# Kernel optimization log

Hardware: AMD Instinct MI355X
Metric: run time of the kernel (lower is better)

The kernel has to match this reference:

```python
import jax, jax.numpy as jnp
import numpy as np

H = 256   # input_size
P = 256   # state_size
BATCH, L = 8, 4096
DT_MIN, DT_MAX = 1e-3, 1e-1
LN_EPS = 1e-5


def _hippo_params():
    # HiPPO-N matrix (num_blocks=1), eigendecomposition in numpy (float64 then cast)
    idx = np.arange(P, dtype=np.float64)
    s = np.sqrt(idx + 0.5)
    A = -np.outer(s, s)
    A = np.tril(A) - np.triu(A, 1)
    np.fill_diagonal(A, -0.5)
    ev, V = np.linalg.eig(A)
    order = np.argsort(ev.real)
    ev, V = ev[order], V[:, order]
    return ev, V


def setup_inputs() -> dict:
    key = jax.random.key(0)
    k_u, = jax.random.split(key, 1)
    ev, V = _hippo_params()
    rng = np.random.default_rng(0)
    log_lambda_real = np.log(-np.clip(ev.real, None, -1e-4)).astype(np.float32)
    lambda_imag = ev.imag.astype(np.float32)
    V_inv = np.linalg.inv(V)
    B_init = rng.standard_normal((P, H)) / np.sqrt(P)
    B_tilde = V_inv @ B_init.astype(np.complex128)
    C_init = rng.standard_normal((H, P)) / np.sqrt(P)
    C_tilde = C_init.astype(np.complex128) @ V
    log_delta = (rng.random(P) * (np.log(DT_MAX) - np.log(DT_MIN)) + np.log(DT_MIN)).astype(np.float32)
    return {
        "u": jax.random.normal(k_u, (BATCH, L, H), dtype=jnp.float32),
        "log_lambda_real": jnp.asarray(log_lambda_real),
        "lambda_imag": jnp.asarray(lambda_imag),
        "B_tilde_real": jnp.asarray(B_tilde.real, dtype=jnp.float32),
        "B_tilde_imag": jnp.asarray(B_tilde.imag, dtype=jnp.float32),
        "C_tilde_real": jnp.asarray(C_tilde.real, dtype=jnp.float32),
        "C_tilde_imag": jnp.asarray(C_tilde.imag, dtype=jnp.float32),
        "log_delta": jnp.asarray(log_delta),
        "gamma": jnp.ones((H,), dtype=jnp.float32),
        "beta": jnp.zeros((H,), dtype=jnp.float32),
    }


def _layernorm(x, gamma, beta):
    mu = jnp.mean(x, axis=-1, keepdims=True)
    var = jnp.mean(jnp.square(x - mu), axis=-1, keepdims=True)
    return (x - mu) * jax.lax.rsqrt(var + LN_EPS) * gamma + beta


def _ssm(h, log_lambda_real, lambda_imag, B_tilde_real, B_tilde_imag,
         C_tilde_real, C_tilde_imag, log_delta):
    # Continuous-time diagonal SSM params
    lam = -jnp.exp(log_lambda_real) + 1j * lambda_imag            # (P,) complex
    B_tilde = B_tilde_real + 1j * B_tilde_imag                     # (P,H)
    C_tilde = C_tilde_real + 1j * C_tilde_imag                     # (H,P)
    delta = jnp.exp(log_delta)                                     # (P,)
    # ZOH discretization (eq. 6 of the S5 paper)
    lambda_bar = jnp.exp(lam * delta)                              # (P,)
    B_bar = ((lambda_bar - 1.0) / lam)[:, None] * B_tilde          # (P,H)
    # Bu_k = B_bar @ u_k  ->  (B,L,P) complex
    Bu = jnp.einsum('blh,ph->blp', h.astype(jnp.complex64), B_bar.astype(jnp.complex64))
    # Parallel associative scan for x_k = lambda_bar * x_{k-1} + Bu_k
    a = jnp.broadcast_to(lambda_bar.astype(jnp.complex64), Bu.shape)
    def combine(c1, c2):
        a1, b1 = c1
        a2, b2 = c2
        return a1 * a2, a2 * b1 + b2
    _, xs = jax.lax.associative_scan(combine, (a, Bu), axis=1)     # (B,L,P)
    # Project back to real output: y = Re(C_tilde @ x)
    y = jnp.einsum('blp,hp->blh', xs, C_tilde.astype(jnp.complex64)).real
    return y


def reference(u, log_lambda_real, lambda_imag, B_tilde_real, B_tilde_imag,
              C_tilde_real, C_tilde_imag, log_delta, gamma, beta):
    # S5Block: pre-LayerNorm -> S5 SSM -> GELU -> residual
    h = _layernorm(u, gamma, beta)
    y = _ssm(h, log_lambda_real, lambda_imag, B_tilde_real, B_tilde_imag,
             C_tilde_real, C_tilde_imag, log_delta)
    return u + jax.nn.gelu(y)
```

## Files before the change

### kernel.cpp

```cpp
#include <hip/hip_runtime.h>
#include <math.h>

#define HDIM 256
#define PDIM 256
#define BATCH 8
#define LSEQ 4096
#define MTOT (BATCH * LSEQ)
#define CHLEN 128
#define NCHUNK 32

typedef __attribute__((ext_vector_type(8))) short bf16x8;
typedef __attribute__((ext_vector_type(4))) float f32x4;

__device__ __forceinline__ unsigned short f2bf(float f) {
    union { float f; unsigned int u; } v; v.f = f;
    unsigned int r = v.u + 0x7FFFu + ((v.u >> 16) & 1u);
    return (unsigned short)(r >> 16);
}
__device__ __forceinline__ float bf2f(unsigned int lo16) {
    union { unsigned int u; float f; } v; v.u = lo16 << 16;
    return v.f;
}

__global__ void prep_k(const float* __restrict__ Br, const float* __restrict__ Bi,
                       const float* __restrict__ Cr, const float* __restrict__ Ci,
                       const float* __restrict__ llr, const float* __restrict__ lim,
                       const float* __restrict__ ldl,
                       unsigned short* __restrict__ W1t, unsigned short* __restrict__ W2t,
                       float* __restrict__ par, float* __restrict__ apw) {
    int p = blockIdx.x, h = threadIdx.x;
    float er = expf(llr[p]);
    float im = lim[p];
    float d  = expf(ldl[p]);
    float zr = -er * d, zi = im * d;
    float ea = expf(zr);
    float ar = ea * cosf(zi), ai = ea * sinf(zi);
    float dr = -er, di = im;
    float den = dr * dr + di * di;
    float nr = ar - 1.0f, ni = ai;
    float cr = (nr * dr + ni * di) / den;
    float ci = (ni * dr - nr * di) / den;
    float br = Br[p * HDIM + h], bi = Bi[p * HDIM + h];
    W1t[(2 * p) * HDIM + h]     = f2bf(cr * br - ci * bi);
    W1t[(2 * p + 1) * HDIM + h] = f2bf(cr * bi + ci * br);
    W2t[h * 512 + 2 * p]     = f2bf(Cr[h * PDIM + p]);
    W2t[h * 512 + 2 * p + 1] = f2bf(-Ci[h * PDIM + p]);
    if (h == 0) {
        par[2 * p]     = ar;
        par[2 * p + 1] = ai;
        float pr = ar, pi = ai;
        apw[2 * p] = pr; apw[2 * p + 1] = pi;
        for (int j = 1; j < CHLEN; j++) {
            float tr = pr * ar - pi * ai;
            float ti = pr * ai + pi * ar;
            pr = tr; pi = ti;
            apw[j * 512 + 2 * p]     = pr;
            apw[j * 512 + 2 * p + 1] = pi;
        }
    }
}

__global__ void ln_k(const float* __restrict__ u, unsigned short* __restrict__ hbf,
                     const float* __restrict__ gamma, const float* __restrict__ beta) {
    __shared__ float gS[HDIM], bS[HDIM];
    int t = threadIdx.x;
    gS[t] = gamma[t]; bS[t] = beta[t];
    int lane = t & 63, wv = t >> 6;
    int row = blockIdx.x * 4 + wv;
    float4 v = *(const float4*)(u + (size_t)row * HDIM + lane * 4);
    float s  = v.x + v.y + v.z + v.w;
    float sq = v.x * v.x + v.y * v.y + v.z * v.z + v.w * v.w;
    #pragma unroll
    for (int o = 1; o < 64; o <<= 1) { s += __shfl_xor(s, o); sq += __shfl_xor(sq, o); }
    float mu = s * (1.0f / HDIM);
    float rs = rsqrtf(sq * (1.0f / HDIM) - mu * mu + 1e-5f);
    __syncthreads();
    int c = lane * 4;
    ushort4 o;
    o.x = f2bf((v.x - mu) * rs * gS[c + 0] + bS[c + 0]);
    o.y = f2bf((v.y - mu) * rs * gS[c + 1] + bS[c + 1]);
    o.z = f2bf((v.z - mu) * rs * gS[c + 2] + bS[c + 2]);
    o.w = f2bf((v.w - mu) * rs * gS[c + 3] + bS[c + 3]);
    *(ushort4*)(hbf + (size_t)row * HDIM + c) = o;
}

__launch_bounds__(256, 2)
__global__ void gemm1_k(const unsigned short* __restrict__ A, const unsigned short* __restrict__ B,
                        unsigned short* __restrict__ Bu, float* __restrict__ last,
                        const float* __restrict__ par, const float* __restrict__ apw) {
    __shared__ union {
        struct { unsigned short A[128 * 32]; unsigned short B[128 * 32]; } st;
        unsigned short C[128 * 128];
    } sm;

    const int t = threadIdx.x;
    const int bn = blockIdx.x, bm = blockIdx.y;
    const int lane = t & 63;
    const int wm = ((t >> 6) & 1) * 64;
    const int wn = ((t >> 6) >> 1) * 64;
    const int srow = t >> 1, skoff = (t & 1) * 16;
    const unsigned short* Ap = A + (size_t)(bm * 128 + srow) * 256 + skoff;
    const unsigned short* Bp = B + (size_t)(bn * 128 + srow) * 256 + skoff;
    const int mrow = lane & 15, kq = (lane >> 4) * 8;

    f32x4 acc[4][4] = {};

    for (int k0 = 0; k0 < 256; k0 += 32) {
        uint4 a0 = *(const uint4*)(Ap + k0);
        uint4 a1 = *(const uint4*)(Ap + k0 + 8);
        uint4 b0 = *(const uint4*)(Bp + k0);
        uint4 b1 = *(const uint4*)(Bp + k0 + 8);
        __syncthreads();
        *(uint4*)&sm.st.A[srow * 32 + skoff]     = a0;
        *(uint4*)&sm.st.A[srow * 32 + skoff + 8] = a1;
        *(uint4*)&sm.st.B[srow * 32 + skoff]     = b0;
        *(uint4*)&sm.st.B[srow * 32 + skoff + 8] = b1;
        __syncthreads();
        bf16x8 fa[4], fb[4];
        #pragma unroll
        for (int i = 0; i < 4; i++) {
            fa[i] = *(const bf16x8*)&sm.st.A[(wm + i * 16 + mrow) * 32 + kq];
            fb[i] = *(const bf16x8*)&sm.st.B[(wn + i * 16 + mrow) * 32 + kq];
        }
        #pragma unroll
        for (int i = 0; i < 4; i++)
            #pragma unroll
            for (int j = 0; j < 4; j++)
                acc[i][j] = __builtin_amdgcn_mfma_f32_16x16x32_bf16(fa[i], fb[j], acc[i][j], 0, 0, 0);
    }

    __syncthreads();
    const int r0 = (lane >> 4) * 4, c0 = lane & 15;
    #pragma unroll
    for (int i = 0; i < 4; i++)
        #pragma unroll
        for (int j = 0; j < 4; j++)
            #pragma unroll
            for (int r = 0; r < 4; r++)
                sm.C[(wm + i * 16 + r0 + r) * 128 + wn + j * 16 + c0] = f2bf(acc[i][j][r]);
    __syncthreads();

    if (t < 64) {
        int pg = bn * 64 + t;
        float ar = par[2 * pg], ai = par[2 * pg + 1];
        float xr = 0.0f, xi = 0.0f;
        unsigned int* Cw = (unsigned int*)sm.C;
        #pragma unroll 8
        for (int s = 0; s < CHLEN; s++) {
            unsigned int v = Cw[s * 64 + t];
            float vr = bf2f(v & 0xFFFFu), vi = bf2f(v >> 16);
            float nr = fmaf(ar, xr, fmaf(-ai, xi, vr));
            float ni = fmaf(ar, xi, fmaf(ai, xr, vi));
            xr = nr; xi = ni;
            Cw[s * 64 + t] = (unsigned int)f2bf(xr) | ((unsigned int)f2bf(xi) << 16);
        }
        *(float2*)(last + (size_t)(bm * 256 + pg) * 2) = make_float2(xr, xi);
    }
    __syncthreads();

    {
        int row = t >> 1, ch = (t & 1) * 64;
        unsigned short* dst = Bu + (size_t)(bm * 128 + row) * 512 + bn * 128 + ch;
        const unsigned short* src = &sm.C[row * 128 + ch];
        #pragma unroll
        for (int q = 0; q < 8; q++)
            *(uint4*)(dst + q * 8) = *(const uint4*)(src + q * 8);
    }
}

__global__ void carry_k(const float* __restrict__ last, float* __restrict__ prefix,
                        const float* __restrict__ apw) {
    int p = threadIdx.x, b = blockIdx.x;
    float Ar = apw[127 * 512 + 2 * p], Ai = apw[127 * 512 + 2 * p + 1];
    float Pr = 0.0f, Pi = 0.0f;
    for (int c = 0; c < NCHUNK; c++) {
        size_t idx = (size_t)((b * NCHUNK + c) * 256 + p) * 2;
        *(float2*)(prefix + idx) = make_float2(Pr, Pi);
        float2 l = *(const float2*)(last + idx);
        float nr = fmaf(Ar, Pr, fmaf(-Ai, Pi, l.x));
        float ni = fmaf(Ar, Pi, fmaf(Ai, Pr, l.y));
        Pr = nr; Pi = ni;
    }
}

__global__ void apply_k(unsigned short* __restrict__ Bu, const float* __restrict__ apw,
                        const float* __restrict__ prefix) {
    int c = blockIdx.x;
    if (c == 0) return;
    int b = blockIdx.y;
    int t = threadIdx.x;
    int k = t & 255;
    int j0 = (t >> 8) * 64;
    float2 P = *(const float2*)(prefix + ((size_t)(b * NCHUNK + c) * 256 + k) * 2);
    unsigned int* q = (unsigned int*)(Bu + ((size_t)b * LSEQ + (size_t)c * CHLEN + j0) * 512) + k;
    const float2* ap = (const float2*)apw + (size_t)j0 * 256 + k;
    #pragma unroll 4
    for (int j = 0; j < 64; j++) {
        float2 a2 = ap[(size_t)j * 256];
        unsigned int v = q[(size_t)j * 256];
        float vr = bf2f(v & 0xFFFFu), vi = bf2f(v >> 16);
        float xr = fmaf(a2.x, P.x, fmaf(-a2.y, P.y, vr));
        float xi = fmaf(a2.x, P.y, fmaf(a2.y, P.x, vi));
        q[(size_t)j * 256] = (unsigned int)f2bf(xr) | ((unsigned int)f2bf(xi) << 16);
    }
}

#define LDK 40
__launch_bounds__(256, 2)
__global__ void gemm2_k(const unsigned short* __restrict__ A, const unsigned short* __restrict__ B,
                        float* __restrict__ out, const float* __restrict__ u) {
    __shared__ unsigned short As[128 * LDK];
    __shared__ unsigned short Bs[128 * LDK];
    const int t = threadIdx.x;
    const int bn = blockIdx.x, bm = blockIdx.y;
    const int lane = t & 63;
    const int wm = ((t >> 6) & 1) * 64;
    const int wn = ((t >> 6) >> 1) * 64;
    const int srow = t >> 1, skoff = (t & 1) * 16;
    const unsigned short* Ap = A + (size_t)(bm * 128 + srow) * 512 + skoff;
    const unsigned short* Bp = B + (size_t)(bn * 128 + srow) * 512 + skoff;
    unsigned short* AsW = &As[srow * LDK + skoff];
    unsigned short* BsW = &Bs[srow * LDK + skoff];
    const int mrow = lane & 15, kq = (lane >> 4) * 8;

    f32x4 acc[4][4] = {};

    for (int k0 = 0; k0 < 512; k0 += 32) {
        uint4 a0 = *(const uint4*)(Ap + k0);
        uint4 a1 = *(const uint4*)(Ap + k0 + 8);
        uint4 b0 = *(const uint4*)(Bp + k0);
        uint4 b1 = *(const uint4*)(Bp + k0 + 8);
        __syncthreads();
        *(uint4*)AsW       = a0;
        *(uint4*)(AsW + 8) = a1;
        *(uint4*)BsW       = b0;
        *(uint4*)(BsW + 8) = b1;
        __syncthreads();
        bf16x8 fa[4], fb[4];
        #pragma unroll
        for (int i = 0; i < 4; i++) {
            fa[i] = *(const bf16x8*)&As[(wm + i * 16 + mrow) * LDK + kq];
            fb[i] = *(const bf16x8*)&Bs[(wn + i * 16 + mrow) * LDK + kq];
        }
        #pragma unroll
        for (int i = 0; i < 4; i++)
            #pragma unroll
            for (int j = 0; j < 4; j++)
                acc[i][j] = __builtin_amdgcn_mfma_f32_16x16x32_bf16(fa[i], fb[j], acc[i][j], 0, 0, 0);
    }

    const int r0 = (lane >> 4) * 4, c0 = lane & 15;
    #pragma unroll
    for (int i = 0; i < 4; i++) {
        #pragma unroll
        for (int r = 0; r < 4; r++) {
            const size_t rowoff = (size_t)(bm * 128 + wm + i * 16 + r0 + r) * 256;
            #pragma unroll
            for (int j = 0; j < 4; j++) {
                const int col = bn * 128 + wn + j * 16 + c0;
                float y = acc[i][j][r];
                float z = 0.7978845608f * fmaf(0.044715f * y * y, y, y);
                float e = __expf(2.0f * z);
                float th = 1.0f - 2.0f / (e + 1.0f);
                out[rowoff + col] = u[rowoff + col] + 0.5f * y * (1.0f + th);
            }
        }
    }
}

extern "C" void kernel_launch(void* const* d_in, const int* in_sizes, int n_in,
                              void* d_out, int out_size, void* d_ws, size_t ws_size,
                              hipStream_t stream) {
    const float* u   = (const float*)d_in[0];
    const float* llr = (const float*)d_in[1];
    const float* lim = (const float*)d_in[2];
    const float* Br  = (const float*)d_in[3];
    const float* Bi  = (const float*)d_in[4];
    const float* Cr  = (const float*)d_in[5];
    const float* Ci  = (const float*)d_in[6];
    const float* ldl = (const float*)d_in[7];
    const float* gam = (const float*)d_in[8];
    const float* bet = (const float*)d_in[9];
    float* out = (float*)d_out;

    float* ws     = (float*)d_ws;
    float* par    = ws;
    float* apw    = ws + 1024;
    float* last   = apw + 128 * 512;
    float* prefix = last + 256 * 256 * 2;
    unsigned short* W1t = (unsigned short*)(prefix + 256 * 256 * 2);
    unsigned short* W2t = W1t + 512 * HDIM;
    unsigned short* hbf = W2t + HDIM * 512;
    unsigned short* Bu  = hbf + (size_t)MTOT * HDIM;

    prep_k<<<PDIM, HDIM, 0, stream>>>(Br, Bi, Cr, Ci, llr, lim, ldl, W1t, W2t, par, apw);
    ln_k<<<MTOT / 4, 256, 0, stream>>>(u, hbf, gam, bet);

    gemm1_k<<<dim3(4, MTOT / 128), 256, 0, stream>>>(hbf, W1t, Bu, last, par, apw);

    carry_k<<<BATCH, PDIM, 0, stream>>>(last, prefix, apw);

    apply_k<<<dim3(NCHUNK, BATCH), 512, 0, stream>>>(Bu, apw, prefix);

    gemm2_k<<<dim3(2, MTOT / 128), 256, 0, stream>>>(Bu, W2t, out, u);
}
```

Baseline: 177.4 us.

## Pre-swizzle GEMM operands into MFMA fragment layout and drop LDS staging

LayerNorm output, both weight matrices, and the chunk-corrected Bu are written directly in per-lane MFMA fragment order. This lets both GEMMs load operands straight from global memory with register double-buffering, with no shared-memory staging or barriers. The apply kernel becomes a fully parallel elementwise pass that writes a separate fragment-ordered buffer, which adds an extra Bu-sized write and read. The carry kernel preloads its chunk values, and the gemm1 scan buffer is padded to reduce LDS bank conflicts.

```diff
diff --git a/kernel.cpp b/kernel.cpp
--- a/kernel.cpp
+++ b/kernel.cpp
@@ -8,6 +8,7 @@
 #define MTOT (BATCH * LSEQ)
 #define CHLEN 128
 #define NCHUNK 32
+#define CPAD 136
 
 typedef __attribute__((ext_vector_type(8))) short bf16x8;
 typedef __attribute__((ext_vector_type(4))) float f32x4;
@@ -21,12 +22,16 @@
     union { unsigned int u; float f; } v; v.u = lo16 << 16;
     return v.f;
 }
+__device__ __forceinline__ unsigned int pack2(float a, float b) {
+    return (unsigned int)f2bf(a) | ((unsigned int)f2bf(b) << 16);
+}
+
 
 __global__ void prep_k(const float* __restrict__ Br, const float* __restrict__ Bi,
                        const float* __restrict__ Cr, const float* __restrict__ Ci,
                        const float* __restrict__ llr, const float* __restrict__ lim,
                        const float* __restrict__ ldl,
-                       unsigned short* __restrict__ W1t, unsigned short* __restrict__ W2t,
+                       unsigned short* __restrict__ W1f, unsigned short* __restrict__ W2f,
                        float* __restrict__ par, float* __restrict__ apw) {
     int p = blockIdx.x, h = threadIdx.x;
     float er = expf(llr[p]);
@@ -41,13 +46,20 @@
     float cr = (nr * dr + ni * di) / den;
     float ci = (ni * dr - nr * di) / den;
     float br = Br[p * HDIM + h], bi = Bi[p * HDIM + h];
-    W1t[(2 * p) * HDIM + h]     = f2bf(cr * br - ci * bi);
-    W1t[(2 * p + 1) * HDIM + h] = f2bf(cr * bi + ci * br);
-    W2t[h * 512 + 2 * p]     = f2bf(Cr[h * PDIM + p]);
-    W2t[h * 512 + 2 * p + 1] = f2bf(-Ci[h * PDIM + p]);
+    {
+        size_t idx = ((size_t)((2 * p) >> 4) * 8 + (h >> 5)) * 512
+                   + ((size_t)((2 * p) & 15) + 16 * ((h & 31) >> 3)) * 8 + (h & 7);
+        W1f[idx]     = f2bf(cr * br - ci * bi);
+        W1f[idx + 8] = f2bf(cr * bi + ci * br);
+    }
+    {
+        size_t idx = ((size_t)(h >> 4) * 16 + (p >> 4)) * 512
+                   + ((size_t)(h & 15) + 16 * (((2 * p) & 31) >> 3)) * 8 + ((2 * p) & 7);
+        W2f[idx]     = f2bf(Cr[h * PDIM + p]);
+        W2f[idx + 1] = f2bf(-Ci[h * PDIM + p]);
+    }
     if (h == 0) {
-        par[2 * p]     = ar;
-        par[2 * p + 1] = ai;
+        par[2 * p] = ar; par[2 * p + 1] = ai;
         float pr = ar, pi = ai;
         apw[2 * p] = pr; apw[2 * p + 1] = pi;
         for (int j = 1; j < CHLEN; j++) {
@@ -57,79 +69,82 @@
             apw[j * 512 + 2 * p]     = pr;
             apw[j * 512 + 2 * p + 1] = pi;
         }
+        par[512 + 2 * p] = pr; par[512 + 2 * p + 1] = pi;
     }
 }
 
 __global__ void ln_k(const float* __restrict__ u, unsigned short* __restrict__ hbf,
                      const float* __restrict__ gamma, const float* __restrict__ beta) {
-    __shared__ float gS[HDIM], bS[HDIM];
-    int t = threadIdx.x;
-    gS[t] = gamma[t]; bS[t] = beta[t];
-    int lane = t & 63, wv = t >> 6;
-    int row = blockIdx.x * 4 + wv;
-    float4 v = *(const float4*)(u + (size_t)row * HDIM + lane * 4);
-    float s  = v.x + v.y + v.z + v.w;
-    float sq = v.x * v.x + v.y * v.y + v.z * v.z + v.w * v.w;
-    #pragma unroll
-    for (int o = 1; o < 64; o <<= 1) { s += __shfl_xor(s, o); sq += __shfl_xor(sq, o); }
-    float mu = s * (1.0f / HDIM);
-    float rs = rsqrtf(sq * (1.0f / HDIM) - mu * mu + 1e-5f);
-    __syncthreads();
-    int c = lane * 4;
-    ushort4 o;
-    o.x = f2bf((v.x - mu) * rs * gS[c + 0] + bS[c + 0]);
-    o.y = f2bf((v.y - mu) * rs * gS[c + 1] + bS[c + 1]);
-    o.z = f2bf((v.z - mu) * rs * gS[c + 2] + bS[c + 2]);
-    o.w = f2bf((v.w - mu) * rs * gS[c + 3] + bS[c + 3]);
-    *(ushort4*)(hbf + (size_t)row * HDIM + c) = o;
+    const int t = threadIdx.x;
+    const int r = t >> 4, s = t & 15;
+    const int mtile = blockIdx.x;
+    const float* up = u + ((size_t)mtile * 16 + r) * 256 + s * 16;
+    float4 v0 = *(const float4*)(up);
+    float4 v1 = *(const float4*)(up + 4);
+    float4 v2 = *(const float4*)(up + 8);
+    float4 v3 = *(const float4*)(up + 12);
+    float va[16];
+    *(float4*)&va[0] = v0; *(float4*)&va[4] = v1; *(float4*)&va[8] = v2; *(float4*)&va[12] = v3;
+    float sum = 0.0f, sq = 0.0f;
+    #pragma unroll
+    for (int q = 0; q < 16; q++) { sum += va[q]; sq += va[q] * va[q]; }
+    #pragma unroll
+    for (int o = 1; o < 16; o <<= 1) { sum += __shfl_xor(sum, o); sq += __shfl_xor(sq, o); }
+    float mu = sum * (1.0f / 256.0f);
+    float rs = rsqrtf(sq * (1.0f / 256.0f) - mu * mu + 1e-5f);
+    const float* gp = gamma + s * 16;
+    const float* bp = beta + s * 16;
+    unsigned int w[8];
+    #pragma unroll
+    for (int q = 0; q < 8; q++)
+        w[q] = pack2((va[2 * q] - mu) * rs * gp[2 * q] + bp[2 * q],
+                     (va[2 * q + 1] - mu) * rs * gp[2 * q + 1] + bp[2 * q + 1]);
+    const int g0 = (s & 1) * 2;
+    unsigned short* dst = hbf + ((size_t)mtile * 8 + (s >> 1)) * 512 + ((size_t)(r) + 16 * g0) * 8;
+    *(uint4*)dst         = make_uint4(w[0], w[1], w[2], w[3]);
+    *(uint4*)(dst + 128) = make_uint4(w[4], w[5], w[6], w[7]);
 }
 
 __launch_bounds__(256, 2)
-__global__ void gemm1_k(const unsigned short* __restrict__ A, const unsigned short* __restrict__ B,
+__global__ void gemm1_k(const unsigned short* __restrict__ hbf, const unsigned short* __restrict__ W1f,
                         unsigned short* __restrict__ Bu, float* __restrict__ last,
-                        const float* __restrict__ par, const float* __restrict__ apw) {
-    __shared__ union {
-        struct { unsigned short A[128 * 32]; unsigned short B[128 * 32]; } st;
-        unsigned short C[128 * 128];
-    } sm;
-
+                        const float* __restrict__ par) {
+    __shared__ unsigned short C[128 * CPAD];
     const int t = threadIdx.x;
     const int bn = blockIdx.x, bm = blockIdx.y;
-    const int lane = t & 63;
-    const int wm = ((t >> 6) & 1) * 64;
-    const int wn = ((t >> 6) >> 1) * 64;
-    const int srow = t >> 1, skoff = (t & 1) * 16;
-    const unsigned short* Ap = A + (size_t)(bm * 128 + srow) * 256 + skoff;
-    const unsigned short* Bp = B + (size_t)(bn * 128 + srow) * 256 + skoff;
-    const int mrow = lane & 15, kq = (lane >> 4) * 8;
+    const int lane = t & 63, w = t >> 6;
+    const unsigned short* Ab = hbf + ((size_t)(bm * 8 + (w & 1) * 4) * 8) * 512 + lane * 8;
+    const unsigned short* Bb = W1f + ((size_t)(bn * 8 + (w >> 1) * 4) * 8) * 512 + lane * 8;
 
     f32x4 acc[4][4] = {};
-
-    for (int k0 = 0; k0 < 256; k0 += 32) {
-        uint4 a0 = *(const uint4*)(Ap + k0);
-        uint4 a1 = *(const uint4*)(Ap + k0 + 8);
-        uint4 b0 = *(const uint4*)(Bp + k0);
-        uint4 b1 = *(const uint4*)(Bp + k0 + 8);
-        __syncthreads();
-        *(uint4*)&sm.st.A[srow * 32 + skoff]     = a0;
-        *(uint4*)&sm.st.A[srow * 32 + skoff + 8] = a1;
-        *(uint4*)&sm.st.B[srow * 32 + skoff]     = b0;
-        *(uint4*)&sm.st.B[srow * 32 + skoff + 8] = b1;
-        __syncthreads();
-        bf16x8 fa[4], fb[4];
-        #pragma unroll
-        for (int i = 0; i < 4; i++) {
-            fa[i] = *(const bf16x8*)&sm.st.A[(wm + i * 16 + mrow) * 32 + kq];
-            fb[i] = *(const bf16x8*)&sm.st.B[(wn + i * 16 + mrow) * 32 + kq];
+    bf16x8 fa[4], fb[4];
+    #pragma unroll
+    for (int i = 0; i < 4; i++) {
+        fa[i] = *(const bf16x8*)(Ab + (size_t)i * 8 * 512);
+        fb[i] = *(const bf16x8*)(Bb + (size_t)i * 8 * 512);
+    }
+    #pragma unroll
+    for (int kt = 0; kt < 8; ++kt) {
+        bf16x8 na[4], nb[4];
+        if (kt < 7) {
+            #pragma unroll
+            for (int i = 0; i < 4; i++) {
+                na[i] = *(const bf16x8*)(Ab + ((size_t)i * 8 + kt + 1) * 512);
+                nb[i] = *(const bf16x8*)(Bb + ((size_t)i * 8 + kt + 1) * 512);
+            }
         }
         #pragma unroll
         for (int i = 0; i < 4; i++)
             #pragma unroll
             for (int j = 0; j < 4; j++)
                 acc[i][j] = __builtin_amdgcn_mfma_f32_16x16x32_bf16(fa[i], fb[j], acc[i][j], 0, 0, 0);
-    }
-
-    __syncthreads();
+        if (kt < 7) {
+            #pragma unroll
+            for (int i = 0; i < 4; i++) { fa[i] = na[i]; fb[i] = nb[i]; }
+        }
+    }
+
+    const int wm = (w & 1) * 64, wn = (w >> 1) * 64;
     const int r0 = (lane >> 4) * 4, c0 = lane & 15;
     #pragma unroll
     for (int i = 0; i < 4; i++)
@@ -137,22 +152,22 @@
         for (int j = 0; j < 4; j++)
             #pragma unroll
             for (int r = 0; r < 4; r++)
-                sm.C[(wm + i * 16 + r0 + r) * 128 + wn + j * 16 + c0] = f2bf(acc[i][j][r]);
+                C[(wm + i * 16 + r0 + r) * CPAD + wn + j * 16 + c0] = f2bf(acc[i][j][r]);
     __syncthreads();
 
     if (t < 64) {
         int pg = bn * 64 + t;
         float ar = par[2 * pg], ai = par[2 * pg + 1];
         float xr = 0.0f, xi = 0.0f;
-        unsigned int* Cw = (unsigned int*)sm.C;
+        unsigned int* Cw = (unsigned int*)C;
         #pragma unroll 8
         for (int s = 0; s < CHLEN; s++) {
-            unsigned int v = Cw[s * 64 + t];
+            unsigned int v = Cw[s * (CPAD / 2) + t];
             float vr = bf2f(v & 0xFFFFu), vi = bf2f(v >> 16);
             float nr = fmaf(ar, xr, fmaf(-ai, xi, vr));
             float ni = fmaf(ar, xi, fmaf(ai, xr, vi));
             xr = nr; xi = ni;
-            Cw[s * 64 + t] = (unsigned int)f2bf(xr) | ((unsigned int)f2bf(xi) << 16);
+            Cw[s * (CPAD / 2) + t] = pack2(xr, xi);
         }
         *(float2*)(last + (size_t)(bm * 256 + pg) * 2) = make_float2(xr, xi);
     }
@@ -161,7 +176,7 @@
     {
         int row = t >> 1, ch = (t & 1) * 64;
         unsigned short* dst = Bu + (size_t)(bm * 128 + row) * 512 + bn * 128 + ch;
-        const unsigned short* src = &sm.C[row * 128 + ch];
+        const unsigned short* src = &C[row * CPAD + ch];
         #pragma unroll
         for (int q = 0; q < 8; q++)
             *(uint4*)(dst + q * 8) = *(const uint4*)(src + q * 8);
@@ -169,86 +184,91 @@
 }
 
 __global__ void carry_k(const float* __restrict__ last, float* __restrict__ prefix,
-                        const float* __restrict__ apw) {
+                        const float* __restrict__ par) {
     int p = threadIdx.x, b = blockIdx.x;
-    float Ar = apw[127 * 512 + 2 * p], Ai = apw[127 * 512 + 2 * p + 1];
+    float Ar = par[512 + 2 * p], Ai = par[512 + 2 * p + 1];
+    float2 L[NCHUNK];
+    #pragma unroll
+    for (int c = 0; c < NCHUNK; c++)
+        L[c] = *(const float2*)(last + ((size_t)(b * NCHUNK + c) * 256 + p) * 2);
     float Pr = 0.0f, Pi = 0.0f;
+    #pragma unroll
     for (int c = 0; c < NCHUNK; c++) {
-        size_t idx = (size_t)((b * NCHUNK + c) * 256 + p) * 2;
-        *(float2*)(prefix + idx) = make_float2(Pr, Pi);
-        float2 l = *(const float2*)(last + idx);
-        float nr = fmaf(Ar, Pr, fmaf(-Ai, Pi, l.x));
-        float ni = fmaf(Ar, Pi, fmaf(Ai, Pr, l.y));
+        *(float2*)(prefix + ((size_t)(b * NCHUNK + c) * 256 + p) * 2) = make_float2(Pr, Pi);
+        float nr = fmaf(Ar, Pr, fmaf(-Ai, Pi, L[c].x));
+        float ni = fmaf(Ar, Pi, fmaf(Ai, Pr, L[c].y));
         Pr = nr; Pi = ni;
     }
 }
 
-__global__ void apply_k(unsigned short* __restrict__ Bu, const float* __restrict__ apw,
-                        const float* __restrict__ prefix) {
-    int c = blockIdx.x;
-    if (c == 0) return;
-    int b = blockIdx.y;
-    int t = threadIdx.x;
-    int k = t & 255;
-    int j0 = (t >> 8) * 64;
-    float2 P = *(const float2*)(prefix + ((size_t)(b * NCHUNK + c) * 256 + k) * 2);
-    unsigned int* q = (unsigned int*)(Bu + ((size_t)b * LSEQ + (size_t)c * CHLEN + j0) * 512) + k;
-    const float2* ap = (const float2*)apw + (size_t)j0 * 256 + k;
-    #pragma unroll 4
-    for (int j = 0; j < 64; j++) {
-        float2 a2 = ap[(size_t)j * 256];
-        unsigned int v = q[(size_t)j * 256];
-        float vr = bf2f(v & 0xFFFFu), vi = bf2f(v >> 16);
-        float xr = fmaf(a2.x, P.x, fmaf(-a2.y, P.y, vr));
-        float xi = fmaf(a2.x, P.y, fmaf(a2.y, P.x, vi));
-        q[(size_t)j * 256] = (unsigned int)f2bf(xr) | ((unsigned int)f2bf(xi) << 16);
-    }
-}
-
-#define LDK 40
+__global__ void apply_k(const unsigned short* __restrict__ Bu, unsigned short* __restrict__ Buf,
+                        const float* __restrict__ apw, const float* __restrict__ prefix) {
+    const size_t gidx = (size_t)blockIdx.x * 256 + threadIdx.x;
+    const int tile = (int)(gidx >> 6), lane_f = (int)(gidx & 63);
+    const int m  = (tile >> 4) * 16 + (lane_f & 15);
+    const int k8 = (tile & 15) * 4 + (lane_f >> 4);
+    const int j  = m & 127;
+    const int bc = m >> 7;
+    uint4 v4 = *(const uint4*)(Bu + (size_t)m * 512 + k8 * 8);
+    float4 f0 = *(const float4*)(apw + (size_t)j * 512 + k8 * 8);
+    float4 f1 = *(const float4*)(apw + (size_t)j * 512 + k8 * 8 + 4);
+    float4 p0 = *(const float4*)(prefix + ((size_t)bc * 256 + k8 * 4) * 2);
+    float4 p1 = *(const float4*)(prefix + ((size_t)bc * 256 + k8 * 4) * 2 + 4);
+    float fv[8], pv[8];
+    *(float4*)&fv[0] = f0; *(float4*)&fv[4] = f1;
+    *(float4*)&pv[0] = p0; *(float4*)&pv[4] = p1;
+    unsigned int vin[4] = {v4.x, v4.y, v4.z, v4.w};
+    unsigned int vout[4];
+    #pragma unroll
+    for (int i = 0; i < 4; i++) {
+        float vr = bf2f(vin[i] & 0xFFFFu), vi = bf2f(vin[i] >> 16);
+        float ar = fv[2 * i], ai = fv[2 * i + 1];
+        float Pr = pv[2 * i], Pi = pv[2 * i + 1];
+        float xr = fmaf(ar, Pr, fmaf(-ai, Pi, vr));
+        float xi = fmaf(ar, Pi, fmaf(ai, Pr, vi));
+        vout[i] = pack2(xr, xi);
+    }
+    *(uint4*)(Buf + gidx * 8) = make_uint4(vout[0], vout[1], vout[2], vout[3]);
+}
+
 __launch_bounds__(256, 2)
-__global__ void gemm2_k(const unsigned short* __restrict__ A, const unsigned short* __restrict__ B,
+__global__ void gemm2_k(const unsigned short* __restrict__ Buf, const unsigned short* __restrict__ W2f,
                         float* __restrict__ out, const float* __restrict__ u) {
-    __shared__ unsigned short As[128 * LDK];
-    __shared__ unsigned short Bs[128 * LDK];
     const int t = threadIdx.x;
     const int bn = blockIdx.x, bm = blockIdx.y;
-    const int lane = t & 63;
-    const int wm = ((t >> 6) & 1) * 64;
-    const int wn = ((t >> 6) >> 1) * 64;
-    const int srow = t >> 1, skoff = (t & 1) * 16;
-    const unsigned short* Ap = A + (size_t)(bm * 128 + srow) * 512 + skoff;
-    const unsigned short* Bp = B + (size_t)(bn * 128 + srow) * 512 + skoff;
-    unsigned short* AsW = &As[srow * LDK + skoff];
-    unsigned short* BsW = &Bs[srow * LDK + skoff];
-    const int mrow = lane & 15, kq = (lane >> 4) * 8;
+    const int lane = t & 63, w = t >> 6;
+    const unsigned short* Ab = Buf + ((size_t)(bm * 8 + (w & 1) * 4) * 16) * 512 + lane * 8;
+    const unsigned short* Bb = W2f + ((size_t)(bn * 8 + (w >> 1) * 4) * 16) * 512 + lane * 8;
 
     f32x4 acc[4][4] = {};
-
-    for (int k0 = 0; k0 < 512; k0 += 32) {
-        uint4 a0 = *(const uint4*)(Ap + k0);
-        uint4 a1 = *(const uint4*)(Ap + k0 + 8);
-        uint4 b0 = *(const uint4*)(Bp + k0);
-        uint4 b1 = *(const uint4*)(Bp + k0 + 8);
-        __syncthreads();
-        *(uint4*)AsW       = a0;
-        *(uint4*)(AsW + 8) = a1;
-        *(uint4*)BsW       = b0;
-        *(uint4*)(BsW + 8) = b1;
-        __syncthreads();
-        bf16x8 fa[4], fb[4];
-        #pragma unroll
-        for (int i = 0; i < 4; i++) {
-            fa[i] = *(const bf16x8*)&As[(wm + i * 16 + mrow) * LDK + kq];
-            fb[i] = *(const bf16x8*)&Bs[(wn + i * 16 + mrow) * LDK + kq];
+    bf16x8 fa[4], fb[4];
+    #pragma unroll
+    for (int i = 0; i < 4; i++) {
+        fa[i] = *(const bf16x8*)(Ab + (size_t)i * 16 * 512);
+        fb[i] = *(const bf16x8*)(Bb + (size_t)i * 16 * 512);
+    }
+    #pragma unroll
+    for (int kt = 0; kt < 16; ++kt) {
+        bf16x8 na[4], nb[4];
+        if (kt < 15) {
+            #pragma unroll
+            for (int i = 0; i < 4; i++) {
+                na[i] = *(const bf16x8*)(Ab + ((size_t)i * 16 + kt + 1) * 512);
+                nb[i] = *(const bf16x8*)(Bb + ((size_t)i * 16 + kt + 1) * 512);
+            }
         }
         #pragma unroll
         for (int i = 0; i < 4; i++)
             #pragma unroll
             for (int j = 0; j < 4; j++)
                 acc[i][j] = __builtin_amdgcn_mfma_f32_16x16x32_bf16(fa[i], fb[j], acc[i][j], 0, 0, 0);
-    }
-
+        if (kt < 15) {
+            #pragma unroll
+            for (int i = 0; i < 4; i++) { fa[i] = na[i]; fb[i] = nb[i]; }
+        }
+    }
+
+    const int wm = (w & 1) * 64, wn = (w >> 1) * 64;
     const int r0 = (lane >> 4) * 4, c0 = lane & 15;
     #pragma unroll
     for (int i = 0; i < 4; i++) {
@@ -288,19 +308,20 @@
     float* apw    = ws + 1024;
     float* last   = apw + 128 * 512;
     float* prefix = last + 256 * 256 * 2;
-    unsigned short* W1t = (unsigned short*)(prefix + 256 * 256 * 2);
-    unsigned short* W2t = W1t + 512 * HDIM;
-    unsigned short* hbf = W2t + HDIM * 512;
+    unsigned short* W1f = (unsigned short*)(prefix + 256 * 256 * 2);
+    unsigned short* W2f = W1f + 512 * HDIM;
+    unsigned short* hbf = W2f + HDIM * 512;
     unsigned short* Bu  = hbf + (size_t)MTOT * HDIM;
-
-    prep_k<<<PDIM, HDIM, 0, stream>>>(Br, Bi, Cr, Ci, llr, lim, ldl, W1t, W2t, par, apw);
-    ln_k<<<MTOT / 4, 256, 0, stream>>>(u, hbf, gam, bet);
-
-    gemm1_k<<<dim3(4, MTOT / 128), 256, 0, stream>>>(hbf, W1t, Bu, last, par, apw);
-
-    carry_k<<<BATCH, PDIM, 0, stream>>>(last, prefix, apw);
-
-    apply_k<<<dim3(NCHUNK, BATCH), 512, 0, stream>>>(Bu, apw, prefix);
-
-    gemm2_k<<<dim3(2, MTOT / 128), 256, 0, stream>>>(Bu, W2t, out, u);
-}
+    unsigned short* Buf = Bu + (size_t)MTOT * 512;
+
+    prep_k<<<PDIM, HDIM, 0, stream>>>(Br, Bi, Cr, Ci, llr, lim, ldl, W1f, W2f, par, apw);
+    ln_k<<<MTOT / 16, 256, 0, stream>>>(u, hbf, gam, bet);
+
+    gemm1_k<<<dim3(4, MTOT / 128), 256, 0, stream>>>(hbf, W1f, Bu, last, par);
+
+    carry_k<<<BATCH, PDIM, 0, stream>>>(last, prefix, par);
+
+    apply_k<<<(MTOT * 512 / 8) / 256, 256, 0, stream>>>(Bu, Buf, apw, prefix);
+
+    gemm2_k<<<dim3(2, MTOT / 128), 256, 0, stream>>>(Buf, W2f, out, u);
+}
```

Result: slower. 191.1 us (+7.7%).
